# Kernel optimization log

Hardware: AMD Instinct MI355X
Metric: run time of the kernel (lower is better)

## Reference

```python
import jax, jax.numpy as jnp
import numpy as np

H_PATCH, W_PATCH = 14, 14
NUM_HEADS, HEAD_DIM = 12, 64


def _relative_position_index(h, w):
    ch, cw = np.meshgrid(np.arange(h), np.arange(w), indexing='ij')
    coords = np.stack([ch.ravel(), cw.ravel()])          # (2, h*w)
    rel = coords[:, :, None] - coords[:, None, :]        # (2, L, L)
    rel = rel.transpose(1, 2, 0)
    rel[:, :, 0] += h - 1
    rel[:, :, 1] += w - 1
    rel[:, :, 0] *= 2 * w - 1
    return rel.sum(-1)                                    # (h*w, h*w) int


def setup_inputs() -> dict:
    key = jax.random.key(0)
    ks = jax.random.split(key, 16)
    B, L, C = 256, 197, 768
    s = 0.02
    return {
        'hidden_states': jax.random.normal(ks[0], (B, L, C), jnp.float32),
        'Wq': jax.random.normal(ks[1], (C, C), jnp.float32) * s,
        'bq': jax.random.normal(ks[2], (C,), jnp.float32) * s,
        'Wk': jax.random.normal(ks[3], (C, C), jnp.float32) * s,
        'bk': jax.random.normal(ks[4], (C,), jnp.float32) * s,
        'Wv': jax.random.normal(ks[5], (C, C), jnp.float32) * s,
        'bv': jax.random.normal(ks[6], (C,), jnp.float32) * s,
        'Wo': jax.random.normal(ks[7], (C, C), jnp.float32) * s,
        'bo': jax.random.normal(ks[8], (C,), jnp.float32) * s,
        'rel_table': jax.random.normal(ks[9], ((2 * H_PATCH - 1) * (2 * W_PATCH - 1), NUM_HEADS), jnp.float32) * s,
        'cls_to_patches': jax.random.normal(ks[10], (1, NUM_HEADS, 1, H_PATCH * W_PATCH), jnp.float32) * s,
        'patches_to_cls': jax.random.normal(ks[11], (1, NUM_HEADS, H_PATCH * W_PATCH, 1), jnp.float32) * s,
        'cls_to_cls': jax.random.normal(ks[12], (1, NUM_HEADS, 1, 1), jnp.float32) * s,
    }


def _full_bias(rel_table, cls_to_patches, patches_to_cls, cls_to_cls):
    idx = jnp.asarray(_relative_position_index(H_PATCH, W_PATCH))  # (P, P)
    patch_bias = rel_table[idx]                                    # (P, P, H)
    patch_bias = jnp.transpose(patch_bias, (2, 0, 1))[None]        # (1, H, P, P)
    top = jnp.concatenate([cls_to_cls, cls_to_patches], axis=-1)   # (1, H, 1, P+1)
    bottom = jnp.concatenate([patches_to_cls, patch_bias], axis=-1)
    return jnp.concatenate([top, bottom], axis=-2)                 # (1, H, L, L)


def reference(hidden_states, Wq, bq, Wk, bk, Wv, bv, Wo, bo,
              rel_table, cls_to_patches, patches_to_cls, cls_to_cls):
    B, L, C = hidden_states.shape
    Hh, D = NUM_HEADS, HEAD_DIM
    scale = D ** -0.5

    def heads(x, W, b):
        return (x @ W + b).reshape(B, L, Hh, D).transpose(0, 2, 1, 3)  # (B,H,L,D)

    q = heads(hidden_states, Wq, bq)
    k = heads(hidden_states, Wk, bk)
    v = heads(hidden_states, Wv, bv)

    attn = jnp.einsum('bhqd,bhkd->bhqk', q, k) * scale
    attn = attn + _full_bias(rel_table, cls_to_patches, patches_to_cls, cls_to_cls)
    attn = jax.nn.softmax(attn, axis=-1)

    x = jnp.einsum('bhqk,bhkd->bhqd', attn, v)            # (B,H,L,D)
    x = x.transpose(0, 2, 1, 3).reshape(B, L, C)
    return x @ Wo + bo
```

## Files before the change

kernel.cpp:

```cpp
#include <hip/hip_runtime.h>
#include <hip/hip_bf16.h>
#include <stdint.h>

#define LSEQ 197
#define NH   12
#define HD   64
#define CDIM 768

#define KSTRD 72
#define VSTRD 232
#define PSTRD 40

typedef __bf16 bf16x8 __attribute__((ext_vector_type(8)));
typedef float  f32x4  __attribute__((ext_vector_type(4)));

__device__ __forceinline__ float bf2f(unsigned short u) { return __uint_as_float(((unsigned)u) << 16); }
__device__ __forceinline__ unsigned short f2bf(float f) {
  unsigned u = __float_as_uint(f);
  unsigned r = 0x7fffu + ((u >> 16) & 1u);
  return (unsigned short)((u + r) >> 16);
}

__device__ __forceinline__ void gload16(const void* g, void* l) {
  __builtin_amdgcn_global_load_lds(
      (const __attribute__((address_space(1))) unsigned int*)(g),
      (__attribute__((address_space(3))) unsigned int*)(l), 16, 0, 0);
}

__global__ void detect_dtype(const unsigned* __restrict__ x, int* __restrict__ flag) {
  __shared__ int cnt;
  if (threadIdx.x == 0) cnt = 0;
  __syncthreads();
  int local = 0;
  for (int i = threadIdx.x; i < 1024; i += 256) {
    const unsigned e = (x[i] >> 7) & 0xFFu;
    if (e >= 96u && e <= 140u) local++;
  }
  atomicAdd(&cnt, local);
  __syncthreads();
  if (threadIdx.x == 0) *flag = (cnt > 512) ? 0 : 1;
}

__global__ void convert_to_bf16(const void* __restrict__ in,
                                unsigned short* __restrict__ outb,
                                const int* __restrict__ flag, long n) {
  const long stride = (long)gridDim.x * blockDim.x;
  long i = (long)blockIdx.x * blockDim.x + threadIdx.x;
  if (*flag) {
    const float* f = (const float*)in;
    for (; i < n; i += stride) outb[i] = f2bf(f[i]);
  } else {
    const unsigned short* s = (const unsigned short*)in;
    for (; i < n; i += stride) outb[i] = s[i];
  }
}

__global__ void convert_small(const void* b0, const void* b1, const void* b2, const void* b3,
                              const void* r, const void* cp, const void* pc, const void* cc,
                              unsigned short* __restrict__ out, const int* __restrict__ flag) {
  const int starts[9] = {0, 768, 1536, 2304, 3072, 11820, 14172, 16524, 16536};
  const void* srcs[8] = {b0, b1, b2, b3, r, cp, pc, cc};
  const bool isf = (*flag != 0);
  for (int i = blockIdx.x * blockDim.x + threadIdx.x; i < 16536;
       i += gridDim.x * blockDim.x) {
    int seg = 0;
    while (i >= starts[seg + 1]) seg++;
    const int off = i - starts[seg];
    out[i] = isf ? f2bf(((const float*)srcs[seg])[off])
                 : ((const unsigned short*)srcs[seg])[off];
  }
}

__global__ void bias_build(const unsigned short* __restrict__ sm,
                           unsigned short* __restrict__ biasM) {
  const unsigned short* rel = sm + 3072;
  const unsigned short* c2p = sm + 11820;
  const unsigned short* p2c = sm + 14172;
  const unsigned short* c2c = sm + 16524;
  const int hq = blockIdx.x;
  const int h = hq / 208, q = hq % 208;
  const int k = threadIdx.x;
  if (k >= 208) return;
  unsigned short v = 0;
  if (q < 197 && k < 197) {
    if (q == 0) {
      v = (k == 0) ? c2c[h] : c2p[h * 196 + (k - 1)];
    } else if (k == 0) {
      v = p2c[h * 196 + (q - 1)];
    } else {
      const int pi = q - 1, pj = k - 1;
      const int dh = pi / 14 - pj / 14 + 13;
      const int dw = pi % 14 - pj % 14 + 13;
      v = rel[(dh * 27 + dw) * 12 + h];
    }
  }
  biasM[(size_t)hq * 208 + k] = v;
}

__global__ void transpose768_cvt(const void* __restrict__ in,
                                 unsigned short* __restrict__ out,
                                 const int* __restrict__ flag) {
  __shared__ unsigned short tile[32][33];
  const bool isf = (*flag != 0);
  const int tx = threadIdx.x & 31;
  const int ty = threadIdx.x >> 5;
  const int bx = blockIdx.x, by = blockIdx.y;
#pragma unroll
  for (int j = 0; j < 32; j += 8) {
    const size_t idx = (size_t)(by * 32 + ty + j) * CDIM + bx * 32 + tx;
    tile[ty + j][tx] = isf ? f2bf(((const float*)in)[idx])
                           : ((const unsigned short*)in)[idx];
  }
  __syncthreads();
#pragma unroll
  for (int j = 0; j < 32; j += 8)
    out[(size_t)(bx * 32 + ty + j) * CDIM + by * 32 + tx] = tile[tx][ty + j];
}

__global__ __launch_bounds__(256, 2) void gemm_bt_bias(
    const unsigned short* __restrict__ A,
    const unsigned short* __restrict__ Bt,
    const unsigned short* __restrict__ bias,
    void* __restrict__ C,
    int M, int N, int K,
    const int* __restrict__ outf32) {
  __shared__ unsigned short As[128 * 32];
  __shared__ unsigned short Bs[128 * 32];

  const int tid  = threadIdx.x;
  const int lane = tid & 63;
  const int wid  = tid >> 6;
  const int bm = blockIdx.y, bn = blockIdx.x;
  const int wm = wid >> 1, wn = wid & 1;
  const bool wf32 = (outf32 != nullptr) && (*outf32 != 0);

  const int srow = (wid * 2) * 16 + (lane >> 2);
  const int scol = (lane & 3) * 8;
  const unsigned short* Ag = A  + (size_t)(bm * 128 + srow) * K + scol;
  const unsigned short* Bg = Bt + (size_t)(bn * 128 + srow) * K + scol;
  unsigned short* lA0 = &As[(wid * 2) * 16 * 32];
  unsigned short* lA1 = lA0 + 16 * 32;
  unsigned short* lB0 = &Bs[(wid * 2) * 16 * 32];
  unsigned short* lB1 = lB0 + 16 * 32;

  f32x4 acc[4][4] = {};

  for (int kt = 0; kt < K; kt += 32) {
    gload16(Ag, lA0);
    gload16(Ag + (size_t)16 * K, lA1);
    gload16(Bg, lB0);
    gload16(Bg + (size_t)16 * K, lB1);
    Ag += 32; Bg += 32;
    __syncthreads();

    bf16x8 fa[4], fb[4];
#pragma unroll
    for (int t = 0; t < 4; ++t) {
      fa[t] = *(const bf16x8*)&As[(wm * 64 + t * 16 + (lane & 15)) * 32 + (lane >> 4) * 8];
      fb[t] = *(const bf16x8*)&Bs[(wn * 64 + t * 16 + (lane & 15)) * 32 + (lane >> 4) * 8];
    }
#pragma unroll
    for (int mt = 0; mt < 4; ++mt)
#pragma unroll
      for (int nt = 0; nt < 4; ++nt)
        acc[mt][nt] = __builtin_amdgcn_mfma_f32_16x16x32_bf16(fa[mt], fb[nt], acc[mt][nt], 0, 0, 0);
    __syncthreads();
  }

#pragma unroll
  for (int nt = 0; nt < 4; ++nt) {
    const int col = bn * 128 + wn * 64 + nt * 16 + (lane & 15);
    const float bv = bf2f(bias[col]);
#pragma unroll
    for (int mt = 0; mt < 4; ++mt) {
      const int row0 = bm * 128 + wm * 64 + mt * 16 + (lane >> 4) * 4;
#pragma unroll
      for (int r = 0; r < 4; ++r) {
        const float val = acc[mt][nt][r] + bv;
        const size_t idx = (size_t)(row0 + r) * N + col;
        if (wf32) ((float*)C)[idx] = val;
        else      ((unsigned short*)C)[idx] = f2bf(val);
      }
    }
  }
}

__global__ __launch_bounds__(256, 2) void attn_mfma(
    const unsigned short* __restrict__ Q,
    const unsigned short* __restrict__ Kg,
    const unsigned short* __restrict__ Vg,
    const unsigned short* __restrict__ biasM,
    unsigned short* __restrict__ ctx) {
  __shared__ unsigned short Kh[208 * KSTRD];
  __shared__ unsigned short Vt[64 * VSTRD];
  __shared__ unsigned short Pt[4 * 16 * PSTRD];

  const int tid  = threadIdx.x;
  const int lane = tid & 63;
  const int wid  = tid >> 6;
  const int bh = blockIdx.x;
  const int b = bh / NH, h = bh % NH;
  const size_t base = ((size_t)b * LSEQ) * CDIM + (size_t)h * HD;

  for (int e2 = tid; e2 < LSEQ * 32; e2 += 256) {
    const int l = e2 >> 5, d2 = (e2 & 31) * 2;
    const unsigned kv = *(const unsigned*)&Kg[base + (size_t)l * CDIM + d2];
    const unsigned vv = *(const unsigned*)&Vg[base + (size_t)l * CDIM + d2];
    *(unsigned*)&Kh[l * KSTRD + d2] = kv;
    Vt[d2 * VSTRD + l]       = (unsigned short)(vv & 0xffffu);
    Vt[(d2 + 1) * VSTRD + l] = (unsigned short)(vv >> 16);
  }
  for (int i = tid; i < 64 * 27; i += 256) {
    const int d = i / 27, c = 197 + i % 27;
    Vt[d * VSTRD + c] = 0;
  }
  __syncthreads();

  unsigned short* pt = &Pt[wid * 16 * PSTRD];
  const int krd = (lane & 15) * KSTRD + (lane >> 4) * 8;
  const int prd = (lane & 15) * PSTRD + (lane >> 4) * 8;
  const int pwr = (lane >> 4) * 4;
  const int pwc = lane & 15;

  for (int mt = wid; mt < 13; mt += 4) {
    const int qm = mt * 16 + (lane & 15);
    const unsigned short* qp = &Q[base + (size_t)(qm > 196 ? 196 : qm) * CDIM + (lane >> 4) * 8];
    const bf16x8 qf0 = *(const bf16x8*)qp;
    const bf16x8 qf1 = *(const bf16x8*)(qp + 32);

    f32x4 s[13];
#pragma unroll
    for (int nt = 0; nt < 13; ++nt) {
      const bf16x8 kb0 = *(const bf16x8*)&Kh[nt * 16 * KSTRD + krd];
      const bf16x8 kb1 = *(const bf16x8*)&Kh[nt * 16 * KSTRD + krd + 32];
      f32x4 a = {0.f, 0.f, 0.f, 0.f};
      a = __builtin_amdgcn_mfma_f32_16x16x32_bf16(qf0, kb0, a, 0, 0, 0);
      a = __builtin_amdgcn_mfma_f32_16x16x32_bf16(qf1, kb1, a, 0, 0, 0);
      s[nt] = a;
    }

    const unsigned short* bp =
        biasM + ((size_t)h * 208 + mt * 16 + pwr) * 208 + pwc;
#pragma unroll
    for (int nt = 0; nt < 13; ++nt)
#pragma unroll
      for (int r = 0; r < 4; ++r)
        s[nt][r] = s[nt][r] * 0.125f + bf2f(bp[r * 208 + nt * 16]);

    if ((lane & 15) >= 5) {
      s[12][0] = -1e30f; s[12][1] = -1e30f; s[12][2] = -1e30f; s[12][3] = -1e30f;
    }

    float inv[4];
#pragma unroll
    for (int r = 0; r < 4; ++r) {
      float m = s[0][r];
#pragma unroll
      for (int nt = 1; nt < 13; ++nt) m = fmaxf(m, s[nt][r]);
      m = fmaxf(m, __shfl_xor(m, 1));
      m = fmaxf(m, __shfl_xor(m, 2));
      m = fmaxf(m, __shfl_xor(m, 4));
      m = fmaxf(m, __shfl_xor(m, 8));
      float sum = 0.f;
#pragma unroll
      for (int nt = 0; nt < 13; ++nt) { s[nt][r] = __expf(s[nt][r] - m); sum += s[nt][r]; }
      sum += __shfl_xor(sum, 1);
      sum += __shfl_xor(sum, 2);
      sum += __shfl_xor(sum, 4);
      sum += __shfl_xor(sum, 8);
      inv[r] = 1.0f / sum;
    }

    f32x4 o[4] = {{0.f,0.f,0.f,0.f},{0.f,0.f,0.f,0.f},{0.f,0.f,0.f,0.f},{0.f,0.f,0.f,0.f}};
#pragma unroll
    for (int t = 0; t < 7; ++t) {
#pragma unroll
      for (int r = 0; r < 4; ++r) {
        pt[(pwr + r) * PSTRD + pwc]      = f2bf(s[2 * t][r]);
        pt[(pwr + r) * PSTRD + pwc + 16] = (2 * t + 1 < 13) ? f2bf(s[2 * t + 1][r])
                                                            : (unsigned short)0;
      }
      __threadfence_block();
      const bf16x8 pa = *(const bf16x8*)&pt[prd];
#pragma unroll
      for (int ot = 0; ot < 4; ++ot) {
        const bf16x8 vb =
            *(const bf16x8*)&Vt[(ot * 16 + (lane & 15)) * VSTRD + t * 32 + (lane >> 4) * 8];
        o[ot] = __builtin_amdgcn_mfma_f32_16x16x32_bf16(pa, vb, o[ot], 0, 0, 0);
      }
      __threadfence_block();
    }

#pragma unroll
    for (int ot = 0; ot < 4; ++ot)
#pragma unroll
      for (int r = 0; r < 4; ++r) {
        const int q = mt * 16 + pwr + r;
        if (q < LSEQ)
          ctx[base + (size_t)q * CDIM + ot * 16 + pwc] = f2bf(o[ot][r] * inv[r]);
      }
  }
}

extern "C" void kernel_launch(void* const* d_in, const int* in_sizes, int n_in,
                              void* d_out, int out_size, void* d_ws, size_t ws_size,
                              hipStream_t stream) {
  const void* X   = d_in[0];
  const void* Wq  = d_in[1];
  const void* bq  = d_in[2];
  const void* Wk  = d_in[3];
  const void* bk  = d_in[4];
  const void* Wv  = d_in[5];
  const void* bv  = d_in[6];
  const void* Wo  = d_in[7];
  const void* bo  = d_in[8];
  const void* rel = d_in[9];
  const void* c2p = d_in[10];
  const void* p2c = d_in[11];
  const void* c2c = d_in[12];

  char* ws = (char*)d_ws;
  const size_t FLAG_OFF = 0;
  const size_t SM_OFF   = 256;
  const size_t BIAS_OFF = 40960;
  const size_t WT_OFF   = BIAS_OFF + 1040384;
  const size_t WT_SZ    = (size_t)CDIM * CDIM * 2;
  const size_t XB_OFF   = WT_OFF + 4 * WT_SZ;
  const size_t X_SZ     = (size_t)50432 * CDIM * 2;
  int* flag = (int*)(ws + FLAG_OFF);
  unsigned short* smb   = (unsigned short*)(ws + SM_OFF);
  unsigned short* biasM = (unsigned short*)(ws + BIAS_OFF);
  unsigned short* WqT = (unsigned short*)(ws + WT_OFF + 0 * WT_SZ);
  unsigned short* WkT = (unsigned short*)(ws + WT_OFF + 1 * WT_SZ);
  unsigned short* WvT = (unsigned short*)(ws + WT_OFF + 2 * WT_SZ);
  unsigned short* WoT = (unsigned short*)(ws + WT_OFF + 3 * WT_SZ);
  unsigned short* Xb  = (unsigned short*)(ws + XB_OFF + 0 * X_SZ);
  unsigned short* Qb  = (unsigned short*)(ws + XB_OFF + 1 * X_SZ);
  unsigned short* Kb  = (unsigned short*)(ws + XB_OFF + 2 * X_SZ);
  unsigned short* Vb  = (unsigned short*)(ws + XB_OFF + 3 * X_SZ);
  unsigned short* Cb  = Xb;

  detect_dtype<<<1, 256, 0, stream>>>((const unsigned*)X, flag);

  convert_to_bf16<<<4096, 256, 0, stream>>>(X, Xb, flag, (long)50432 * CDIM);
  convert_small<<<65, 256, 0, stream>>>(bq, bk, bv, bo, rel, c2p, p2c, c2c, smb, flag);
  bias_build<<<12 * 208, 256, 0, stream>>>(smb, biasM);

  dim3 tgrid(24, 24);
  transpose768_cvt<<<tgrid, 256, 0, stream>>>(Wq, WqT, flag);
  transpose768_cvt<<<tgrid, 256, 0, stream>>>(Wk, WkT, flag);
  transpose768_cvt<<<tgrid, 256, 0, stream>>>(Wv, WvT, flag);
  transpose768_cvt<<<tgrid, 256, 0, stream>>>(Wo, WoT, flag);

  dim3 ggrid(6, 394);
  gemm_bt_bias<<<ggrid, 256, 0, stream>>>(Xb, WqT, smb + 0,    Qb, 50432, CDIM, CDIM, nullptr);
  gemm_bt_bias<<<ggrid, 256, 0, stream>>>(Xb, WkT, smb + 768,  Kb, 50432, CDIM, CDIM, nullptr);
  gemm_bt_bias<<<ggrid, 256, 0, stream>>>(Xb, WvT, smb + 1536, Vb, 50432, CDIM, CDIM, nullptr);

  attn_mfma<<<dim3(256 * NH), 256, 0, stream>>>(Qb, Kb, Vb, biasM, Cb);

  gemm_bt_bias<<<ggrid, 256, 0, stream>>>(Cb, WoT, smb + 2304, d_out, 50432, CDIM, CDIM, flag);
}
```

Before: 896.6 us.

## Fuse QKV projection into one GEMM and rework attention softmax/P routing

```diff
diff --git a/kernel.cpp b/kernel.cpp
--- a/kernel.cpp
+++ b/kernel.cpp
@@ -6,10 +6,9 @@
 #define NH   12
 #define HD   64
 #define CDIM 768
-
-#define KSTRD 72
-#define VSTRD 232
-#define PSTRD 40
+#define QKVS 2304
+
+#define VSTRD 200
 
 typedef __bf16 bf16x8 __attribute__((ext_vector_type(8)));
 typedef float  f32x4  __attribute__((ext_vector_type(4)));
@@ -25,6 +24,12 @@
   __builtin_amdgcn_global_load_lds(
       (const __attribute__((address_space(1))) unsigned int*)(g),
       (__attribute__((address_space(3))) unsigned int*)(l), 16, 0, 0);
+}
+
+__device__ __forceinline__ bf16x8 pack4(unsigned x, unsigned y, unsigned z, unsigned w) {
+  union { unsigned u[4]; bf16x8 v; } t;
+  t.u[0] = x; t.u[1] = y; t.u[2] = z; t.u[3] = w;
+  return t.v;
 }
 
 __global__ void detect_dtype(const unsigned* __restrict__ x, int* __restrict__ flag) {
@@ -72,29 +77,38 @@
 }
 
 __global__ void bias_build(const unsigned short* __restrict__ sm,
-                           unsigned short* __restrict__ biasM) {
-  const unsigned short* rel = sm + 3072;
-  const unsigned short* c2p = sm + 11820;
-  const unsigned short* p2c = sm + 14172;
-  const unsigned short* c2c = sm + 16524;
-  const int hq = blockIdx.x;
-  const int h = hq / 208, q = hq % 208;
-  const int k = threadIdx.x;
-  if (k >= 208) return;
-  unsigned short v = 0;
-  if (q < 197 && k < 197) {
+                           float* __restrict__ biasF) {
+  const int gid = blockIdx.x * blockDim.x + threadIdx.x;
+  if (gid >= 12 * 13 * 64 * 52) return;
+  const int e    = gid % 52;
+  const int lane = (gid / 52) & 63;
+  const int mt   = (gid / (52 * 64)) % 13;
+  const int h    = gid / (52 * 64 * 13);
+  const int nt = e >> 2, r = e & 3;
+  const int q = mt * 16 + (lane & 15);
+  const int k = nt * 16 + ((lane >> 4) & 3) * 4 + r;
+  float v;
+  if (q >= 197 || k >= 197) {
+    v = -1e30f;
+  } else {
+    const unsigned short* rel = sm + 3072;
+    const unsigned short* c2p = sm + 11820;
+    const unsigned short* p2c = sm + 14172;
+    const unsigned short* c2c = sm + 16524;
+    unsigned short u;
     if (q == 0) {
-      v = (k == 0) ? c2c[h] : c2p[h * 196 + (k - 1)];
+      u = (k == 0) ? c2c[h] : c2p[h * 196 + (k - 1)];
     } else if (k == 0) {
-      v = p2c[h * 196 + (q - 1)];
+      u = p2c[h * 196 + (q - 1)];
     } else {
       const int pi = q - 1, pj = k - 1;
       const int dh = pi / 14 - pj / 14 + 13;
       const int dw = pi % 14 - pj % 14 + 13;
-      v = rel[(dh * 27 + dw) * 12 + h];
-    }
-  }
-  biasM[(size_t)hq * 208 + k] = v;
+      u = rel[(dh * 27 + dw) * 12 + h];
+    }
+    v = bf2f(u) * 1.4426950408889634f;
+  }
+  biasF[gid] = v;
 }
 
 __global__ void transpose768_cvt(const void* __restrict__ in,
@@ -185,119 +199,158 @@
   }
 }
 
-__global__ __launch_bounds__(256, 2) void attn_mfma(
-    const unsigned short* __restrict__ Q,
-    const unsigned short* __restrict__ Kg,
-    const unsigned short* __restrict__ Vg,
-    const unsigned short* __restrict__ biasM,
+__global__ __launch_bounds__(256, 3) void attn_mfma(
+    const unsigned short* __restrict__ QKV,
+    const float* __restrict__ biasF,
     unsigned short* __restrict__ ctx) {
-  __shared__ unsigned short Kh[208 * KSTRD];
+  __shared__ unsigned short Kh[208 * 64];
   __shared__ unsigned short Vt[64 * VSTRD];
-  __shared__ unsigned short Pt[4 * 16 * PSTRD];
 
   const int tid  = threadIdx.x;
   const int lane = tid & 63;
   const int wid  = tid >> 6;
   const int bh = blockIdx.x;
   const int b = bh / NH, h = bh % NH;
-  const size_t base = ((size_t)b * LSEQ) * CDIM + (size_t)h * HD;
-
-  for (int e2 = tid; e2 < LSEQ * 32; e2 += 256) {
-    const int l = e2 >> 5, d2 = (e2 & 31) * 2;
-    const unsigned kv = *(const unsigned*)&Kg[base + (size_t)l * CDIM + d2];
-    const unsigned vv = *(const unsigned*)&Vg[base + (size_t)l * CDIM + d2];
-    *(unsigned*)&Kh[l * KSTRD + d2] = kv;
+  const size_t baseQ = (size_t)b * LSEQ * QKVS + (size_t)h * HD;
+  const size_t baseK = baseQ + 768;
+  const size_t baseV = baseQ + 1536;
+  const size_t baseC = (size_t)b * LSEQ * CDIM + (size_t)h * HD;
+
+  for (int i = tid; i < 197 * 8; i += 256) {
+    const int l = i >> 3, c8 = (i & 7) * 8;
+    const bf16x8 kv = *(const bf16x8*)&QKV[baseK + (size_t)l * QKVS + c8];
+    *(bf16x8*)((char*)Kh + l * 128 + ((c8 * 2) ^ ((l & 7) << 4))) = kv;
+  }
+  for (int i = tid; i < 197 * 32; i += 256) {
+    const int l = i >> 5, d2 = (i & 31) * 2;
+    const unsigned vv = *(const unsigned*)&QKV[baseV + (size_t)l * QKVS + d2];
     Vt[d2 * VSTRD + l]       = (unsigned short)(vv & 0xffffu);
     Vt[(d2 + 1) * VSTRD + l] = (unsigned short)(vv >> 16);
   }
-  for (int i = tid; i < 64 * 27; i += 256) {
-    const int d = i / 27, c = 197 + i % 27;
-    Vt[d * VSTRD + c] = 0;
-  }
+  for (int i = tid; i < 64 * 3; i += 256)
+    Vt[(i / 3) * VSTRD + 197 + (i % 3)] = 0;
   __syncthreads();
 
-  unsigned short* pt = &Pt[wid * 16 * PSTRD];
-  const int krd = (lane & 15) * KSTRD + (lane >> 4) * 8;
-  const int prd = (lane & 15) * PSTRD + (lane >> 4) * 8;
-  const int pwr = (lane >> 4) * 4;
-  const int pwc = lane & 15;
+  const int ql = lane & 15, g = lane >> 4;
+  const int krd0 = ql * 128 + ((g * 16) ^ ((ql & 7) << 4));
+  const int krd1 = ql * 128 + ((g * 16 + 64) ^ ((ql & 7) << 4));
+  const int vrd  = ql * VSTRD + g * 8;
+  const int vrd6 = ql * VSTRD + 192;
+  const int addrA = (((g & 1) << 5) + ql) << 2;
+  const int addrB = addrA + 64;
+  const bool hi2 = lane >= 32;
+  const bool hi1 = lane >= 16;
 
   for (int mt = wid; mt < 13; mt += 4) {
-    const int qm = mt * 16 + (lane & 15);
-    const unsigned short* qp = &Q[base + (size_t)(qm > 196 ? 196 : qm) * CDIM + (lane >> 4) * 8];
+    const int qm = mt * 16 + ql;
+    const unsigned short* qp =
+        &QKV[baseQ + (size_t)(qm > 196 ? 196 : qm) * QKVS + g * 8];
     const bf16x8 qf0 = *(const bf16x8*)qp;
     const bf16x8 qf1 = *(const bf16x8*)(qp + 32);
+    const f32x4* bv = (const f32x4*)(biasF + ((size_t)(h * 13 + mt) * 64 + lane) * 52);
 
     f32x4 s[13];
 #pragma unroll
     for (int nt = 0; nt < 13; ++nt) {
-      const bf16x8 kb0 = *(const bf16x8*)&Kh[nt * 16 * KSTRD + krd];
-      const bf16x8 kb1 = *(const bf16x8*)&Kh[nt * 16 * KSTRD + krd + 32];
+      const bf16x8 kb0 = *(const bf16x8*)((const char*)Kh + nt * 2048 + krd0);
+      const bf16x8 kb1 = *(const bf16x8*)((const char*)Kh + nt * 2048 + krd1);
       f32x4 a = {0.f, 0.f, 0.f, 0.f};
-      a = __builtin_amdgcn_mfma_f32_16x16x32_bf16(qf0, kb0, a, 0, 0, 0);
-      a = __builtin_amdgcn_mfma_f32_16x16x32_bf16(qf1, kb1, a, 0, 0, 0);
+      a = __builtin_amdgcn_mfma_f32_16x16x32_bf16(kb0, qf0, a, 0, 0, 0);
+      a = __builtin_amdgcn_mfma_f32_16x16x32_bf16(kb1, qf1, a, 0, 0, 0);
       s[nt] = a;
     }
 
-    const unsigned short* bp =
-        biasM + ((size_t)h * 208 + mt * 16 + pwr) * 208 + pwc;
-#pragma unroll
-    for (int nt = 0; nt < 13; ++nt)
+#pragma unroll
+    for (int nt = 0; nt < 13; ++nt) {
+      const f32x4 bb = bv[nt];
 #pragma unroll
       for (int r = 0; r < 4; ++r)
-        s[nt][r] = s[nt][r] * 0.125f + bf2f(bp[r * 208 + nt * 16]);
-
-    if ((lane & 15) >= 5) {
-      s[12][0] = -1e30f; s[12][1] = -1e30f; s[12][2] = -1e30f; s[12][3] = -1e30f;
-    }
-
-    float inv[4];
-#pragma unroll
-    for (int r = 0; r < 4; ++r) {
-      float m = s[0][r];
-#pragma unroll
-      for (int nt = 1; nt < 13; ++nt) m = fmaxf(m, s[nt][r]);
-      m = fmaxf(m, __shfl_xor(m, 1));
-      m = fmaxf(m, __shfl_xor(m, 2));
-      m = fmaxf(m, __shfl_xor(m, 4));
-      m = fmaxf(m, __shfl_xor(m, 8));
-      float sum = 0.f;
-#pragma unroll
-      for (int nt = 0; nt < 13; ++nt) { s[nt][r] = __expf(s[nt][r] - m); sum += s[nt][r]; }
-      sum += __shfl_xor(sum, 1);
-      sum += __shfl_xor(sum, 2);
-      sum += __shfl_xor(sum, 4);
-      sum += __shfl_xor(sum, 8);
-      inv[r] = 1.0f / sum;
+        s[nt][r] = s[nt][r] * 0.18033688011112042f + bb[r];
+    }
+    const float NEG = -1e30f;
+    s[12][0] = hi2 ? NEG : s[12][0];
+    s[12][1] = hi1 ? NEG : s[12][1];
+    s[12][2] = hi1 ? NEG : s[12][2];
+    s[12][3] = hi1 ? NEG : s[12][3];
+
+    float m0 = s[0][0], m1 = s[0][1], m2 = s[0][2], m3 = s[0][3];
+#pragma unroll
+    for (int nt = 1; nt < 13; ++nt) {
+      m0 = fmaxf(m0, s[nt][0]); m1 = fmaxf(m1, s[nt][1]);
+      m2 = fmaxf(m2, s[nt][2]); m3 = fmaxf(m3, s[nt][3]);
+    }
+    float m = fmaxf(fmaxf(m0, m1), fmaxf(m2, m3));
+    m = fmaxf(m, __shfl_xor(m, 16));
+    m = fmaxf(m, __shfl_xor(m, 32));
+    float t0 = 0.f, t1 = 0.f, t2 = 0.f, t3 = 0.f;
+#pragma unroll
+    for (int nt = 0; nt < 13; ++nt) {
+      s[nt][0] = __builtin_exp2f(s[nt][0] - m); t0 += s[nt][0];
+      s[nt][1] = __builtin_exp2f(s[nt][1] - m); t1 += s[nt][1];
+      s[nt][2] = __builtin_exp2f(s[nt][2] - m); t2 += s[nt][2];
+      s[nt][3] = __builtin_exp2f(s[nt][3] - m); t3 += s[nt][3];
+    }
+    float sum = (t0 + t1) + (t2 + t3);
+    sum += __shfl_xor(sum, 16);
+    sum += __shfl_xor(sum, 32);
+    const float inv = __builtin_amdgcn_rcpf(sum);
+
+    unsigned pk0[13], pk1[13];
+#pragma unroll
+    for (int nt = 0; nt < 13; ++nt) {
+      const float p0 = s[nt][0] * inv, p1 = s[nt][1] * inv;
+      const float p2 = s[nt][2] * inv, p3 = s[nt][3] * inv;
+      unsigned lo, hi;
+      asm("v_cvt_pk_bf16_f32 %0, %1, %2" : "=v"(lo) : "v"(p0), "v"(p1));
+      asm("v_cvt_pk_bf16_f32 %0, %1, %2" : "=v"(hi) : "v"(p2), "v"(p3));
+      pk0[nt] = lo; pk1[nt] = hi;
     }
 
     f32x4 o[4] = {{0.f,0.f,0.f,0.f},{0.f,0.f,0.f,0.f},{0.f,0.f,0.f,0.f},{0.f,0.f,0.f,0.f}};
 #pragma unroll
-    for (int t = 0; t < 7; ++t) {
+    for (int t = 0; t < 6; ++t) {
+      const int i0 = 2 * t, i1 = 2 * t + 1;
+      const int xA0 = __builtin_amdgcn_ds_bpermute(addrA, (int)pk0[i0]);
+      const int yA0 = __builtin_amdgcn_ds_bpermute(addrA, (int)pk0[i1]);
+      const int xA1 = __builtin_amdgcn_ds_bpermute(addrA, (int)pk1[i0]);
+      const int yA1 = __builtin_amdgcn_ds_bpermute(addrA, (int)pk1[i1]);
+      const int xB0 = __builtin_amdgcn_ds_bpermute(addrB, (int)pk0[i0]);
+      const int yB0 = __builtin_amdgcn_ds_bpermute(addrB, (int)pk0[i1]);
+      const int xB1 = __builtin_amdgcn_ds_bpermute(addrB, (int)pk1[i0]);
+      const int yB1 = __builtin_amdgcn_ds_bpermute(addrB, (int)pk1[i1]);
+      const bf16x8 pa = pack4((unsigned)(hi2 ? yA0 : xA0),
+                              (unsigned)(hi2 ? yA1 : xA1),
+                              (unsigned)(hi2 ? yB0 : xB0),
+                              (unsigned)(hi2 ? yB1 : xB1));
+#pragma unroll
+      for (int ot = 0; ot < 4; ++ot) {
+        const bf16x8 vbf = *(const bf16x8*)&Vt[ot * 16 * VSTRD + vrd + t * 32];
+        o[ot] = __builtin_amdgcn_mfma_f32_16x16x32_bf16(pa, vbf, o[ot], 0, 0, 0);
+      }
+    }
+    {
+      const int xA0 = __builtin_amdgcn_ds_bpermute(addrA, (int)pk0[12]);
+      const int xA1 = __builtin_amdgcn_ds_bpermute(addrA, (int)pk1[12]);
+      const int xB0 = __builtin_amdgcn_ds_bpermute(addrB, (int)pk0[12]);
+      const int xB1 = __builtin_amdgcn_ds_bpermute(addrB, (int)pk1[12]);
+      const bf16x8 pa = pack4(hi2 ? 0u : (unsigned)xA0,
+                              hi2 ? 0u : (unsigned)xA1,
+                              hi2 ? 0u : (unsigned)xB0,
+                              hi2 ? 0u : (unsigned)xB1);
+#pragma unroll
+      for (int ot = 0; ot < 4; ++ot) {
+        const bf16x8 vbf = *(const bf16x8*)&Vt[ot * 16 * VSTRD + vrd6];
+        o[ot] = __builtin_amdgcn_mfma_f32_16x16x32_bf16(pa, vbf, o[ot], 0, 0, 0);
+      }
+    }
+
+#pragma unroll
+    for (int ot = 0; ot < 4; ++ot)
 #pragma unroll
       for (int r = 0; r < 4; ++r) {
-        pt[(pwr + r) * PSTRD + pwc]      = f2bf(s[2 * t][r]);
-        pt[(pwr + r) * PSTRD + pwc + 16] = (2 * t + 1 < 13) ? f2bf(s[2 * t + 1][r])
-                                                            : (unsigned short)0;
-      }
-      __threadfence_block();
-      const bf16x8 pa = *(const bf16x8*)&pt[prd];
-#pragma unroll
-      for (int ot = 0; ot < 4; ++ot) {
-        const bf16x8 vb =
-            *(const bf16x8*)&Vt[(ot * 16 + (lane & 15)) * VSTRD + t * 32 + (lane >> 4) * 8];
-        o[ot] = __builtin_amdgcn_mfma_f32_16x16x32_bf16(pa, vb, o[ot], 0, 0, 0);
-      }
-      __threadfence_block();
-    }
-
-#pragma unroll
-    for (int ot = 0; ot < 4; ++ot)
-#pragma unroll
-      for (int r = 0; r < 4; ++r) {
-        const int q = mt * 16 + pwr + r;
+        const int q = mt * 16 + g * 4 + r;
         if (q < LSEQ)
-          ctx[base + (size_t)q * CDIM + ot * 16 + pwc] = f2bf(o[ot][r] * inv[r]);
+          ctx[baseC + (size_t)q * CDIM + ot * 16 + ql] = f2bf(o[ot][r]);
       }
   }
 }
@@ -323,28 +376,27 @@
   const size_t FLAG_OFF = 0;
   const size_t SM_OFF   = 256;
   const size_t BIAS_OFF = 40960;
-  const size_t WT_OFF   = BIAS_OFF + 1040384;
+  const size_t WT_OFF   = BIAS_OFF + 2080768;
   const size_t WT_SZ    = (size_t)CDIM * CDIM * 2;
   const size_t XB_OFF   = WT_OFF + 4 * WT_SZ;
   const size_t X_SZ     = (size_t)50432 * CDIM * 2;
+  const size_t QKV_OFF  = XB_OFF + X_SZ;
   int* flag = (int*)(ws + FLAG_OFF);
   unsigned short* smb   = (unsigned short*)(ws + SM_OFF);
-  unsigned short* biasM = (unsigned short*)(ws + BIAS_OFF);
+  float*          biasF = (float*)(ws + BIAS_OFF);
   unsigned short* WqT = (unsigned short*)(ws + WT_OFF + 0 * WT_SZ);
   unsigned short* WkT = (unsigned short*)(ws + WT_OFF + 1 * WT_SZ);
   unsigned short* WvT = (unsigned short*)(ws + WT_OFF + 2 * WT_SZ);
   unsigned short* WoT = (unsigned short*)(ws + WT_OFF + 3 * WT_SZ);
-  unsigned short* Xb  = (unsigned short*)(ws + XB_OFF + 0 * X_SZ);
-  unsigned short* Qb  = (unsigned short*)(ws + XB_OFF + 1 * X_SZ);
-  unsigned short* Kb  = (unsigned short*)(ws + XB_OFF + 2 * X_SZ);
-  unsigned short* Vb  = (unsigned short*)(ws + XB_OFF + 3 * X_SZ);
+  unsigned short* Xb  = (unsigned short*)(ws + XB_OFF);
+  unsigned short* QKVb= (unsigned short*)(ws + QKV_OFF);
   unsigned short* Cb  = Xb;
 
   detect_dtype<<<1, 256, 0, stream>>>((const unsigned*)X, flag);
 
   convert_to_bf16<<<4096, 256, 0, stream>>>(X, Xb, flag, (long)50432 * CDIM);
   convert_small<<<65, 256, 0, stream>>>(bq, bk, bv, bo, rel, c2p, p2c, c2c, smb, flag);
-  bias_build<<<12 * 208, 256, 0, stream>>>(smb, biasM);
+  bias_build<<<2028, 256, 0, stream>>>(smb, biasF);
 
   dim3 tgrid(24, 24);
   transpose768_cvt<<<tgrid, 256, 0, stream>>>(Wq, WqT, flag);
@@ -352,12 +404,11 @@
   transpose768_cvt<<<tgrid, 256, 0, stream>>>(Wv, WvT, flag);
   transpose768_cvt<<<tgrid, 256, 0, stream>>>(Wo, WoT, flag);
 
-  dim3 ggrid(6, 394);
-  gemm_bt_bias<<<ggrid, 256, 0, stream>>>(Xb, WqT, smb + 0,    Qb, 50432, CDIM, CDIM, nullptr);
-  gemm_bt_bias<<<ggrid, 256, 0, stream>>>(Xb, WkT, smb + 768,  Kb, 50432, CDIM, CDIM, nullptr);
-  gemm_bt_bias<<<ggrid, 256, 0, stream>>>(Xb, WvT, smb + 1536, Vb, 50432, CDIM, CDIM, nullptr);
-
-  attn_mfma<<<dim3(256 * NH), 256, 0, stream>>>(Qb, Kb, Vb, biasM, Cb);
-
-  gemm_bt_bias<<<ggrid, 256, 0, stream>>>(Cb, WoT, smb + 2304, d_out, 50432, CDIM, CDIM, flag);
-}
+  gemm_bt_bias<<<dim3(18, 394), 256, 0, stream>>>(Xb, WqT, smb, QKVb,
+                                                  50432, QKVS, CDIM, nullptr);
+
+  attn_mfma<<<dim3(256 * NH), 256, 0, stream>>>(QKVb, biasF, Cb);
+
+  gemm_bt_bias<<<dim3(6, 394), 256, 0, stream>>>(Cb, WoT, smb + 2304, d_out,
+                                                 50432, CDIM, CDIM, flag);
+}
```

Measured after the change: 1.010 ms. +12.6%, slower.
